# Performance work log

Hardware: AMD Instinct MI355X
Metric: run time of the kernel (lower is better)

## Reference

```python
import jax, jax.numpy as jnp
import numpy as np

N_IN = 1000000   # non-empty input octants at depth d
N_OUT = 125000   # parent octants at depth d-1 (stride-2 downsample)
C_IN = 96
C_OUT = 192
K = 8            # 2x2x2 kernel -> 8 children per parent
BN_EPS = 1e-5


def setup_inputs() -> dict:
    key = jax.random.key(0)
    k1, k2, k3, k4 = jax.random.split(key, 4)
    data = jax.random.normal(k1, (N_IN, C_IN), dtype=jnp.float32)
    # child-neighbor table: index into input rows; <0 would mean empty child
    neigh = jax.random.randint(k2, (N_OUT, K), 0, N_IN, dtype=jnp.int64)
    # OctreeConv weights [K, Cin, Cout] + bias, BatchNorm affine params
    fan_in = K * C_IN
    weights = jax.random.normal(k3, (K, C_IN, C_OUT), dtype=jnp.float32) / np.sqrt(fan_in)
    bias = jax.random.normal(k4, (C_OUT,), dtype=jnp.float32) * 0.01
    gamma = jnp.ones((C_OUT,), dtype=jnp.float32)
    beta = jnp.zeros((C_OUT,), dtype=jnp.float32)
    return {"data": data, "weights": weights, "bias": bias,
            "gamma": gamma, "beta": beta, "neigh": neigh}


def reference(data, weights, bias, gamma, beta, neigh):
    # --- OctreeConv, kernel 2x2x2, stride 2, nempty=True ---
    valid = neigh >= 0                                   # [M, K]
    idx = jnp.clip(neigh, 0)                             # safe gather index
    gathered = data[idx]                                 # [M, K, Cin]
    gathered = jnp.where(valid[:, :, None], gathered, 0.0)
    out = jnp.einsum('mkc,kcd->md', gathered, weights) + bias  # [M, Cout]
    # --- BatchNorm1d over node dim (training-mode batch stats) ---
    mean = jnp.mean(out, axis=0)
    var = jnp.var(out, axis=0)                           # biased variance
    out = (out - mean) * jax.lax.rsqrt(var + BN_EPS) * gamma + beta
    return out
```

## Files before the change

kernel.cpp:

```cpp
#include <hip/hip_runtime.h>

#define M_OUT   125000
#define CIN     96
#define COUT    192
#define KOCT    8
#define MT      128
#define LDA     104
#define LDB     104
#define BN_EPS  1e-5f

#define WS_SCALE_OFF 384
#define WS_WT_BYTE   4096

typedef __attribute__((ext_vector_type(8))) short bf16x8;
typedef __attribute__((ext_vector_type(4))) float f32x4;

__device__ __forceinline__ unsigned short f2bf(float f) {
    unsigned int u = __float_as_uint(f);
    u += 0x7FFF + ((u >> 16) & 1);
    return (unsigned short)(u >> 16);
}

__device__ __forceinline__ unsigned int pack2(float a, float b) {
    unsigned int ua = __float_as_uint(a);
    unsigned int ub = __float_as_uint(b);
    ua += 0x7FFF + ((ua >> 16) & 1);
    ub += 0x7FFF + ((ub >> 16) & 1);
    return (ua >> 16) | (ub & 0xFFFF0000u);
}

__global__ void prep_kernel(const float* __restrict__ W, float* __restrict__ ws_f,
                            unsigned short* __restrict__ wt) {
    int gid = blockIdx.x * blockDim.x + threadIdx.x;
    if (gid < 384) ws_f[gid] = 0.0f;
    if (gid < KOCT * COUT * LDA) {
        int c = gid % LDA;
        int rest = gid / LDA;
        int n = rest % COUT;
        int k = rest / COUT;
        float v = (c < CIN) ? W[(k * CIN + c) * COUT + n] : 0.0f;
        wt[gid] = f2bf(v);
    }
}

__global__ __launch_bounds__(256, 2)
void conv_kernel(const float* __restrict__ data,
                 const int* __restrict__ neigh,
                 const float* __restrict__ bias,
                 const unsigned short* __restrict__ wt,
                 float* __restrict__ out,
                 float* __restrict__ gsum) {
    __shared__ unsigned short As[MT * LDA];
    __shared__ unsigned short Bs[COUT * LDB];
    __shared__ int   idxs[MT * KOCT];
    __shared__ float stats[2 * COUT];

    const int t    = threadIdx.x;
    const int wave = t >> 6;
    const int lane = t & 63;
    const int quad = lane >> 4;
    const int l15  = lane & 15;
    const int wr   = wave >> 1;
    const int wc   = wave & 1;
    const int m0   = blockIdx.x * MT;

    {
        int r  = t >> 1;
        int gm = m0 + r;
        int4 v;
        if (gm < M_OUT) {
            v = *reinterpret_cast<const int4*>(neigh + gm * 8 + (t & 1) * 4);
        } else {
            v.x = v.y = v.z = v.w = -1;
        }
        *reinterpret_cast<int4*>(idxs + t * 4) = v;
        for (int i = t; i < 2 * COUT; i += 256) stats[i] = 0.0f;
    }

    const f32x4 vzero = {0.f, 0.f, 0.f, 0.f};
    f32x4 acc[4][6];
#pragma unroll
    for (int i = 0; i < 4; ++i)
#pragma unroll
        for (int j = 0; j < 6; ++j) acc[i][j] = vzero;

    __syncthreads();

    for (int k = 0; k < KOCT; ++k) {
#pragma unroll
        for (int j = 0; j < 12; ++j) {
            int lin = j * 256 + t;
            int row = lin / 24;
            int f4  = lin - row * 24;
            int idx = idxs[row * 8 + k];
            unsigned int lo = 0u, hi = 0u;
            if (idx >= 0) {
                float4 v = *reinterpret_cast<const float4*>(data + (size_t)idx * CIN + f4 * 4);
                lo = pack2(v.x, v.y);
                hi = pack2(v.z, v.w);
            }
            uint2 p; p.x = lo; p.y = hi;
            *reinterpret_cast<uint2*>(&As[row * LDA + f4 * 4]) = p;
        }
        {
            const uint4* src = reinterpret_cast<const uint4*>(wt + k * COUT * LDB);
            uint4* dst = reinterpret_cast<uint4*>(Bs);
#pragma unroll
            for (int j = 0; j < 10; ++j) {
                int i = j * 256 + t;
                if (i < (COUT * LDB * 2) / 16) dst[i] = src[i];
            }
        }
        __syncthreads();

#pragma unroll
        for (int ks = 0; ks < 3; ++ks) {
            bf16x8 af[4], bfr[6];
#pragma unroll
            for (int rt = 0; rt < 4; ++rt) {
                int row = wr * 64 + rt * 16 + l15;
                af[rt] = *reinterpret_cast<const bf16x8*>(&As[row * LDA + ks * 32 + quad * 8]);
            }
#pragma unroll
            for (int ct = 0; ct < 6; ++ct) {
                int n = wc * 96 + ct * 16 + l15;
                bfr[ct] = *reinterpret_cast<const bf16x8*>(&Bs[n * LDB + ks * 32 + quad * 8]);
            }
#pragma unroll
            for (int rt = 0; rt < 4; ++rt)
#pragma unroll
                for (int ct = 0; ct < 6; ++ct)
                    acc[rt][ct] = __builtin_amdgcn_mfma_f32_16x16x32_bf16(
                        af[rt], bfr[ct], acc[rt][ct], 0, 0, 0);
        }
        __syncthreads();
    }

#pragma unroll
    for (int ct = 0; ct < 6; ++ct) {
        int col = wc * 96 + ct * 16 + l15;
        float b = bias[col];
        float s1 = 0.f, s2 = 0.f;
#pragma unroll
        for (int rt = 0; rt < 4; ++rt) {
#pragma unroll
            for (int r = 0; r < 4; ++r) {
                int gm = m0 + wr * 64 + rt * 16 + quad * 4 + r;
                if (gm < M_OUT) {
                    float v = acc[rt][ct][r] + b;
                    out[(size_t)gm * COUT + col] = v;
                    s1 += v;
                    s2 += v * v;
                }
            }
        }
        atomicAdd(&stats[col], s1);
        atomicAdd(&stats[COUT + col], s2);
    }
    __syncthreads();
    for (int i = t; i < COUT; i += 256) {
        atomicAdd(&gsum[i], stats[i]);
        atomicAdd(&gsum[COUT + i], stats[COUT + i]);
    }
}

__global__ void finalize_kernel(const float* __restrict__ gsum,
                                const float* __restrict__ gamma,
                                const float* __restrict__ beta,
                                float* __restrict__ ss) {
    int c = threadIdx.x;
    if (c < COUT) {
        float inv_m = 1.0f / (float)M_OUT;
        float mean = gsum[c] * inv_m;
        float var  = gsum[COUT + c] * inv_m - mean * mean;
        float rstd = rsqrtf(var + BN_EPS);
        float sc   = gamma[c] * rstd;
        ss[c]        = sc;
        ss[COUT + c] = beta[c] - mean * sc;
    }
}

__global__ void norm_kernel(float* __restrict__ out, const float* __restrict__ ss) {
    __shared__ float s_scale[COUT], s_shift[COUT];
    for (int i = threadIdx.x; i < COUT; i += blockDim.x) {
        s_scale[i] = ss[i];
        s_shift[i] = ss[COUT + i];
    }
    __syncthreads();
    const int total4 = M_OUT * COUT / 4;
    int stride = gridDim.x * blockDim.x;
    for (int i = blockIdx.x * blockDim.x + threadIdx.x; i < total4; i += stride) {
        float4 v = reinterpret_cast<float4*>(out)[i];
        int c4 = (i % (COUT / 4)) * 4;
        v.x = v.x * s_scale[c4 + 0] + s_shift[c4 + 0];
        v.y = v.y * s_scale[c4 + 1] + s_shift[c4 + 1];
        v.z = v.z * s_scale[c4 + 2] + s_shift[c4 + 2];
        v.w = v.w * s_scale[c4 + 3] + s_shift[c4 + 3];
        reinterpret_cast<float4*>(out)[i] = v;
    }
}

extern "C" void kernel_launch(void* const* d_in, const int* in_sizes, int n_in,
                              void* d_out, int out_size, void* d_ws, size_t ws_size,
                              hipStream_t stream) {
    const float* data  = (const float*)d_in[0];
    const float* W     = (const float*)d_in[1];
    const float* bias  = (const float*)d_in[2];
    const float* gamma = (const float*)d_in[3];
    const float* beta  = (const float*)d_in[4];
    const int*   neigh = (const int*)d_in[5];
    float* out  = (float*)d_out;
    float* ws_f = (float*)d_ws;
    unsigned short* wt = (unsigned short*)((char*)d_ws + WS_WT_BYTE);

    prep_kernel<<<(KOCT * COUT * LDA + 255) / 256, 256, 0, stream>>>(W, ws_f, wt);

    int grid1 = (M_OUT + MT - 1) / MT;
    conv_kernel<<<grid1, 256, 0, stream>>>(data, neigh, bias, wt, out, ws_f);

    finalize_kernel<<<1, 192, 0, stream>>>(ws_f, gamma, beta, ws_f + WS_SCALE_OFF);

    norm_kernel<<<4096, 256, 0, stream>>>(out, ws_f + WS_SCALE_OFF);
}
```

Measured before the change: 659.5 us.

## Gather A directly into MFMA registers and double-buffer weights via async LDS loads

The conv kernel now uses 512 threads per 256-row tile. Each wave gathers its own rows' input features straight into registers in MFMA fragment layout, which removes the A shared-memory tile and the neighbor index table. Weight slices are double-buffered in LDS with global_load_lds, and the next octant's gather is issued before the current MFMA phase, so memory latency can overlap compute. Per-column stats are reduced with wave shuffles before the LDS atomics; in exchange the kernel holds more registers and each lane issues uncoalesced 32-byte gather loads.

```diff
diff --git a/kernel.cpp b/kernel.cpp
--- a/kernel.cpp
+++ b/kernel.cpp
@@ -4,7 +4,7 @@
 #define CIN     96
 #define COUT    192
 #define KOCT    8
-#define MT      128
+#define MT      256
 #define LDA     104
 #define LDB     104
 #define BN_EPS  1e-5f
@@ -27,6 +27,22 @@
     ua += 0x7FFF + ((ua >> 16) & 1);
     ub += 0x7FFF + ((ub >> 16) & 1);
     return (ua >> 16) | (ub & 0xFFFF0000u);
+}
+
+__device__ __forceinline__ bf16x8 pack8(const float4 h0, const float4 h1) {
+    union { unsigned int u[4]; bf16x8 v; } r;
+    r.u[0] = pack2(h0.x, h0.y);
+    r.u[1] = pack2(h0.z, h0.w);
+    r.u[2] = pack2(h1.x, h1.y);
+    r.u[3] = pack2(h1.z, h1.w);
+    return r.v;
+}
+
+__device__ __forceinline__ int sel8(const int4 a, const int4 b, int k) {
+    switch (k & 7) {
+        case 0: return a.x; case 1: return a.y; case 2: return a.z; case 3: return a.w;
+        case 4: return b.x; case 5: return b.y; case 6: return b.z; default: return b.w;
+    }
 }
 
 __global__ void prep_kernel(const float* __restrict__ W, float* __restrict__ ws_f,
@@ -43,16 +59,14 @@
     }
 }
 
-__global__ __launch_bounds__(256, 2)
+__global__ __launch_bounds__(512, 2)
 void conv_kernel(const float* __restrict__ data,
                  const int* __restrict__ neigh,
                  const float* __restrict__ bias,
                  const unsigned short* __restrict__ wt,
                  float* __restrict__ out,
                  float* __restrict__ gsum) {
-    __shared__ unsigned short As[MT * LDA];
-    __shared__ unsigned short Bs[COUT * LDB];
-    __shared__ int   idxs[MT * KOCT];
+    __shared__ __align__(16) unsigned short Bs[2][COUT * LDB];
     __shared__ float stats[2 * COUT];
 
     const int t    = threadIdx.x;
@@ -60,92 +74,118 @@
     const int lane = t & 63;
     const int quad = lane >> 4;
     const int l15  = lane & 15;
-    const int wr   = wave >> 1;
-    const int wc   = wave & 1;
     const int m0   = blockIdx.x * MT;
 
-    {
-        int r  = t >> 1;
-        int gm = m0 + r;
-        int4 v;
+    for (int i = t; i < 2 * COUT; i += 512) stats[i] = 0.0f;
+
+    int4 nid[2][2];
+#pragma unroll
+    for (int rt = 0; rt < 2; ++rt) {
+        int gm = m0 + wave * 32 + rt * 16 + l15;
         if (gm < M_OUT) {
-            v = *reinterpret_cast<const int4*>(neigh + gm * 8 + (t & 1) * 4);
+            nid[rt][0] = *reinterpret_cast<const int4*>(neigh + (size_t)gm * 8);
+            nid[rt][1] = *reinterpret_cast<const int4*>(neigh + (size_t)gm * 8 + 4);
         } else {
-            v.x = v.y = v.z = v.w = -1;
-        }
-        *reinterpret_cast<int4*>(idxs + t * 4) = v;
-        for (int i = t; i < 2 * COUT; i += 256) stats[i] = 0.0f;
-    }
-
-    const f32x4 vzero = {0.f, 0.f, 0.f, 0.f};
-    f32x4 acc[4][6];
-#pragma unroll
-    for (int i = 0; i < 4; ++i)
-#pragma unroll
-        for (int j = 0; j < 6; ++j) acc[i][j] = vzero;
-
+            nid[rt][0] = make_int4(-1, -1, -1, -1);
+            nid[rt][1] = make_int4(-1, -1, -1, -1);
+        }
+    }
+
+    f32x4 acc[2][12];
+    const f32x4 vz = {0.f, 0.f, 0.f, 0.f};
+#pragma unroll
+    for (int i = 0; i < 2; ++i)
+#pragma unroll
+        for (int j = 0; j < 12; ++j) acc[i][j] = vz;
+
+    float4 ar[12];
+    bf16x8 af[2][2][3];
+
+    auto gather = [&](int k) {
+#pragma unroll
+        for (int rt = 0; rt < 2; ++rt) {
+            int idx = sel8(nid[rt][0], nid[rt][1], k);
+            const float* p = data + (size_t)idx * CIN + quad * 8;
+#pragma unroll
+            for (int ks = 0; ks < 3; ++ks)
+#pragma unroll
+                for (int h = 0; h < 2; ++h) {
+                    float4 v = {0.f, 0.f, 0.f, 0.f};
+                    if (idx >= 0) v = *reinterpret_cast<const float4*>(p + ks * 32 + h * 4);
+                    ar[(rt * 3 + ks) * 2 + h] = v;
+                }
+        }
+    };
+    auto packA = [&](int buf) {
+#pragma unroll
+        for (int rt = 0; rt < 2; ++rt)
+#pragma unroll
+            for (int ks = 0; ks < 3; ++ks)
+                af[buf][rt][ks] = pack8(ar[(rt * 3 + ks) * 2], ar[(rt * 3 + ks) * 2 + 1]);
+    };
+    auto stageB = [&](int k, int buf) {
+        const char* src = (const char*)wt + (size_t)k * (COUT * LDB * 2);
+        char* dst = (char*)&Bs[buf][0];
+#pragma unroll
+        for (int j = 0; j < 5; ++j) {
+            int chunk = wave + 8 * j;
+            if (chunk < 39) {
+                __builtin_amdgcn_global_load_lds(
+                    (const __attribute__((address_space(1))) unsigned int*)(src + chunk * 1024 + lane * 16),
+                    (__attribute__((address_space(3))) unsigned int*)(dst + chunk * 1024 + lane * 16),
+                    16, 0, 0);
+            }
+        }
+    };
+    auto mfmaPhase = [&](int kbuf, int bbuf) {
+#pragma unroll
+        for (int ks = 0; ks < 3; ++ks)
+#pragma unroll
+            for (int h = 0; h < 2; ++h) {
+                bf16x8 bfr[6];
+#pragma unroll
+                for (int c = 0; c < 6; ++c) {
+                    int n = h * 96 + c * 16 + l15;
+                    bfr[c] = *reinterpret_cast<const bf16x8*>(&Bs[bbuf][n * LDB + ks * 32 + quad * 8]);
+                }
+#pragma unroll
+                for (int rt = 0; rt < 2; ++rt)
+#pragma unroll
+                    for (int c = 0; c < 6; ++c)
+                        acc[rt][h * 6 + c] = __builtin_amdgcn_mfma_f32_16x16x32_bf16(
+                            af[kbuf][rt][ks], bfr[c], acc[rt][h * 6 + c], 0, 0, 0);
+            }
+    };
+
+    gather(0);
+    stageB(0, 0);
+    packA(0);
     __syncthreads();
 
+#pragma unroll
     for (int k = 0; k < KOCT; ++k) {
-#pragma unroll
-        for (int j = 0; j < 12; ++j) {
-            int lin = j * 256 + t;
-            int row = lin / 24;
-            int f4  = lin - row * 24;
-            int idx = idxs[row * 8 + k];
-            unsigned int lo = 0u, hi = 0u;
-            if (idx >= 0) {
-                float4 v = *reinterpret_cast<const float4*>(data + (size_t)idx * CIN + f4 * 4);
-                lo = pack2(v.x, v.y);
-                hi = pack2(v.z, v.w);
-            }
-            uint2 p; p.x = lo; p.y = hi;
-            *reinterpret_cast<uint2*>(&As[row * LDA + f4 * 4]) = p;
-        }
-        {
-            const uint4* src = reinterpret_cast<const uint4*>(wt + k * COUT * LDB);
-            uint4* dst = reinterpret_cast<uint4*>(Bs);
-#pragma unroll
-            for (int j = 0; j < 10; ++j) {
-                int i = j * 256 + t;
-                if (i < (COUT * LDB * 2) / 16) dst[i] = src[i];
-            }
-        }
+        const int cb = k & 1;
+        if (k < KOCT - 1) {
+            gather(k + 1);
+            stageB(k + 1, cb ^ 1);
+        }
+        __builtin_amdgcn_sched_barrier(0);
+        mfmaPhase(cb, cb);
+        __builtin_amdgcn_sched_barrier(0);
+        if (k < KOCT - 1) packA(cb ^ 1);
         __syncthreads();
-
-#pragma unroll
-        for (int ks = 0; ks < 3; ++ks) {
-            bf16x8 af[4], bfr[6];
-#pragma unroll
-            for (int rt = 0; rt < 4; ++rt) {
-                int row = wr * 64 + rt * 16 + l15;
-                af[rt] = *reinterpret_cast<const bf16x8*>(&As[row * LDA + ks * 32 + quad * 8]);
-            }
-#pragma unroll
-            for (int ct = 0; ct < 6; ++ct) {
-                int n = wc * 96 + ct * 16 + l15;
-                bfr[ct] = *reinterpret_cast<const bf16x8*>(&Bs[n * LDB + ks * 32 + quad * 8]);
-            }
-#pragma unroll
-            for (int rt = 0; rt < 4; ++rt)
-#pragma unroll
-                for (int ct = 0; ct < 6; ++ct)
-                    acc[rt][ct] = __builtin_amdgcn_mfma_f32_16x16x32_bf16(
-                        af[rt], bfr[ct], acc[rt][ct], 0, 0, 0);
-        }
-        __syncthreads();
-    }
-
-#pragma unroll
-    for (int ct = 0; ct < 6; ++ct) {
-        int col = wc * 96 + ct * 16 + l15;
+    }
+
+#pragma unroll
+    for (int ct = 0; ct < 12; ++ct) {
+        int col = ct * 16 + l15;
         float b = bias[col];
         float s1 = 0.f, s2 = 0.f;
 #pragma unroll
-        for (int rt = 0; rt < 4; ++rt) {
+        for (int rt = 0; rt < 2; ++rt) {
 #pragma unroll
             for (int r = 0; r < 4; ++r) {
-                int gm = m0 + wr * 64 + rt * 16 + quad * 4 + r;
+                int gm = m0 + wave * 32 + rt * 16 + quad * 4 + r;
                 if (gm < M_OUT) {
                     float v = acc[rt][ct][r] + b;
                     out[(size_t)gm * COUT + col] = v;
@@ -154,11 +194,15 @@
                 }
             }
         }
-        atomicAdd(&stats[col], s1);
-        atomicAdd(&stats[COUT + col], s2);
+        s1 += __shfl_xor(s1, 16); s2 += __shfl_xor(s2, 16);
+        s1 += __shfl_xor(s1, 32); s2 += __shfl_xor(s2, 32);
+        if (quad == 0) {
+            atomicAdd(&stats[col], s1);
+            atomicAdd(&stats[COUT + col], s2);
+        }
     }
     __syncthreads();
-    for (int i = t; i < COUT; i += 256) {
+    for (int i = t; i < COUT; i += 512) {
         atomicAdd(&gsum[i], stats[i]);
         atomicAdd(&gsum[COUT + i], stats[COUT + i]);
     }
@@ -216,7 +260,7 @@
     prep_kernel<<<(KOCT * COUT * LDA + 255) / 256, 256, 0, stream>>>(W, ws_f, wt);
 
     int grid1 = (M_OUT + MT - 1) / MT;
-    conv_kernel<<<grid1, 256, 0, stream>>>(data, neigh, bias, wt, out, ws_f);
+    conv_kernel<<<grid1, 512, 0, stream>>>(data, neigh, bias, wt, out, ws_f);
 
     finalize_kernel<<<1, 192, 0, stream>>>(ws_f, gamma, beta, ws_f + WS_SCALE_OFF);
 
```

Measured after the change: 595.6 us. -9.7%, faster.
